# Optimization experiments

Hardware: AMD Instinct MI355X
Metric: run time of the kernel (lower is better)

The kernel has to match this reference:

```python
import jax, jax.numpy as jnp
import numpy as np

B, N, C, F = 8, 2048, 256, 128

def setup_inputs() -> dict:
    key = jax.random.key(0)
    ks = jax.random.split(key, 5)
    s = 0.02
    return {
        "x": jax.random.normal(ks[0], (B, N, C), dtype=jnp.float32),
        "Wf": jax.random.normal(ks[1], (C, F), dtype=jnp.float32) * s,
        "bf": jnp.zeros((F,), jnp.float32),
        "Wg": jax.random.normal(ks[2], (C, F), dtype=jnp.float32) * s,
        "bg": jnp.zeros((F,), jnp.float32),
        "Wh": jax.random.normal(ks[3], (C, F), dtype=jnp.float32) * s,
        "bh": jnp.zeros((F,), jnp.float32),
        "Wv": jax.random.normal(ks[4], (F, F), dtype=jnp.float32) * s,
        "bv": jnp.zeros((F,), jnp.float32),
    }

def reference(x, Wf, bf, Wg, bg, Wh, bh, Wv, bv):
    # 1x1 Conv1D == pointwise dense projection
    fx = x @ Wf + bf            # [B, N, F]
    gx = x @ Wg + bg            # [B, N, F]
    hx = x @ Wh + bh            # [B, N, F]
    # alpha = softmax(fx @ gx^T) over last axis -> [B, N, N]
    alpha = jax.nn.softmax(jnp.einsum('bnf,bmf->bnm', fx, gx), axis=-1)
    # o = hx^T @ alpha -> [B, F, N]
    o = jnp.einsum('bnf,bnm->bfm', hx, alpha)
    # faithful to original: RESHAPE (not transpose) to [B, N, F]
    o = o.reshape(B, N, F)
    return o @ Wv + bv          # [B, N, F]
```

## Files before the change

kernel.cpp:

```cpp
#include <hip/hip_runtime.h>
#include <hip/hip_bf16.h>


constexpr int Bb = 8, Nn = 2048, Cc = 256, Ff = 128;
constexpr long BNF = (long)Bb * Nn * Ff;
constexpr long BN  = (long)Bb * Nn;

typedef __bf16 bf16x8 __attribute__((ext_vector_type(8)));
typedef float  f32x4  __attribute__((ext_vector_type(4)));

__device__ inline unsigned short f2bf(float x) {
    unsigned u = __float_as_uint(x);
    unsigned r = (u + 0x7fffu + ((u >> 16) & 1u)) >> 16;
    return (unsigned short)r;
}
__device__ inline float bf2f(unsigned short h) {
    return __uint_as_float(((unsigned)h) << 16);
}


__global__ __launch_bounds__(256) void k_prepw(
    const float* __restrict__ W0, const float* __restrict__ W1,
    const float* __restrict__ W2,
    ushort* __restrict__ wth, ushort* __restrict__ wtl)
{
    __shared__ float ls[64][132];
    const float* W = (blockIdx.y == 0) ? W0 : (blockIdx.y == 1) ? W1 : W2;
    const int k0 = blockIdx.x * 64;
    const int t = threadIdx.x;
    const float4* src = (const float4*)(W + (size_t)k0 * 128);
    #pragma unroll
    for (int i = 0; i < 8; ++i) {
        int idx = t + 256 * i;
        int r = idx >> 5, c4 = idx & 31;
        *(float4*)&ls[r][c4 * 4] = src[idx];
    }
    __syncthreads();
    const int f = t >> 1, half = t & 1;
    __align__(16) ushort hb[32], lb[32];
    #pragma unroll
    for (int j = 0; j < 32; ++j) {
        float v = ls[half * 32 + j][f];
        ushort h = f2bf(v);
        hb[j] = h;
        lb[j] = f2bf(v - bf2f(h));
    }
    size_t base = ((size_t)blockIdx.y * 128 + f) * 256 + k0 + half * 32;
    #pragma unroll
    for (int j = 0; j < 4; ++j) {
        *(uint4*)&wth[base + j * 8] = *(const uint4*)&hb[j * 8];
        *(uint4*)&wtl[base + j * 8] = *(const uint4*)&lb[j * 8];
    }
}

__global__ __launch_bounds__(256) void k_prepwv(
    const float* __restrict__ Wv,
    ushort* __restrict__ wvth, ushort* __restrict__ wvtl)
{
    __shared__ float ls[64][132];
    const int k0 = blockIdx.x * 64;
    const int t = threadIdx.x;
    const float4* src = (const float4*)(Wv + (size_t)k0 * 128);
    #pragma unroll
    for (int i = 0; i < 8; ++i) {
        int idx = t + 256 * i;
        int r = idx >> 5, c4 = idx & 31;
        *(float4*)&ls[r][c4 * 4] = src[idx];
    }
    __syncthreads();
    const int f = t >> 1, half = t & 1;
    __align__(16) ushort hb[32], lb[32];
    #pragma unroll
    for (int j = 0; j < 32; ++j) {
        float v = ls[half * 32 + j][f];
        ushort h = f2bf(v);
        hb[j] = h;
        lb[j] = f2bf(v - bf2f(h));
    }
    size_t base = (size_t)f * 128 + k0 + half * 32;
    #pragma unroll
    for (int j = 0; j < 4; ++j) {
        *(uint4*)&wvth[base + j * 8] = *(const uint4*)&hb[j * 8];
        *(uint4*)&wvtl[base + j * 8] = *(const uint4*)&lb[j * 8];
    }
}

__global__ __launch_bounds__(512) void k_projm2(
    const float* __restrict__ x,
    const ushort* __restrict__ wth, const ushort* __restrict__ wtl,
    const float* __restrict__ b0, const float* __restrict__ b1,
    const float* __restrict__ b2,
    ushort* __restrict__ fxh, ushort* __restrict__ fxl,
    ushort* __restrict__ gxh, ushort* __restrict__ gxl,
    float* __restrict__ hxt)
{
    __shared__ ushort xsh[64][264], xsl[64][264];
    __shared__ float pmf[64][132];
    ushort (*pm)[136] = (ushort(*)[136])pmf;

    const int t = threadIdx.x;
    const long row0 = (long)blockIdx.x * 64;
    const int wid = t >> 6, lane = t & 63;
    const int wy = wid & 1, wx = wid >> 1;
    const int col = lane & 15, quad = lane >> 4;

    {
        #pragma unroll
        for (int i = 0; i < 8; ++i) {
            int idx = t + 512 * i;
            int r = idx >> 6, c4 = idx & 63;
            float4 v = *(const float4*)&x[(row0 + r) * 256 + c4 * 4];
            ushort4 h, l;
            h.x = f2bf(v.x); l.x = f2bf(v.x - bf2f(h.x));
            h.y = f2bf(v.y); l.y = f2bf(v.y - bf2f(h.y));
            h.z = f2bf(v.z); l.z = f2bf(v.z - bf2f(h.z));
            h.w = f2bf(v.w); l.w = f2bf(v.w - bf2f(h.w));
            *(ushort4*)&xsh[r][c4 * 4] = h;
            *(ushort4*)&xsl[r][c4 * 4] = l;
        }
    }
    __syncthreads();

    for (int y = 0; y < 3; ++y) {
        const ushort* Wh = wth + (size_t)y * 128 * 256;
        const ushort* Wl = wtl + (size_t)y * 128 * 256;
        const float* bias = (y == 0) ? b0 : (y == 1) ? b1 : b2;

        f32x4 acc[2][2];
        #pragma unroll
        for (int i = 0; i < 2; ++i)
            #pragma unroll
            for (int j = 0; j < 2; ++j) acc[i][j] = (f32x4){0.f, 0.f, 0.f, 0.f};

        #pragma unroll
        for (int kk = 0; kk < 8; ++kk) {
            const int ko = kk * 32 + quad * 8;
            bf16x8 ah[2], al[2], bh[2], bl[2];
            #pragma unroll
            for (int tn = 0; tn < 2; ++tn) {
                int r = wy * 32 + tn * 16 + col;
                ah[tn] = *(const bf16x8*)&xsh[r][ko];
                al[tn] = *(const bf16x8*)&xsl[r][ko];
            }
            #pragma unroll
            for (int tf = 0; tf < 2; ++tf) {
                int f = wx * 32 + tf * 16 + col;
                bh[tf] = *(const bf16x8*)&Wh[(size_t)f * 256 + ko];
                bl[tf] = *(const bf16x8*)&Wl[(size_t)f * 256 + ko];
            }
            #pragma unroll
            for (int tn = 0; tn < 2; ++tn)
                #pragma unroll
                for (int tf = 0; tf < 2; ++tf) {
                    acc[tn][tf] = __builtin_amdgcn_mfma_f32_16x16x32_bf16(ah[tn], bh[tf], acc[tn][tf], 0, 0, 0);
                    acc[tn][tf] = __builtin_amdgcn_mfma_f32_16x16x32_bf16(ah[tn], bl[tf], acc[tn][tf], 0, 0, 0);
                    acc[tn][tf] = __builtin_amdgcn_mfma_f32_16x16x32_bf16(al[tn], bh[tf], acc[tn][tf], 0, 0, 0);
                }
        }

        float v[2][2][4];
        #pragma unroll
        for (int tf = 0; tf < 2; ++tf) {
            float bb = bias[wx * 32 + tf * 16 + col];
            #pragma unroll
            for (int tn = 0; tn < 2; ++tn)
                #pragma unroll
                for (int r = 0; r < 4; ++r) v[tn][tf][r] = acc[tn][tf][r] + bb;
        }

        if (y == 2) {
            float* ob = hxt + (row0 >> 11) * (size_t)128 * 2048;
            int n0 = (int)(row0 & 2047);
            #pragma unroll
            for (int tn = 0; tn < 2; ++tn) {
                int n = n0 + wy * 32 + tn * 16 + quad * 4;
                #pragma unroll
                for (int tf = 0; tf < 2; ++tf) {
                    int f = wx * 32 + tf * 16 + col;
                    f32x4 vv = {v[tn][tf][0], v[tn][tf][1], v[tn][tf][2], v[tn][tf][3]};
                    *(f32x4*)&ob[(size_t)f * 2048 + n] = vv;
                }
            }
        } else {
            ushort* oh = (y == 0) ? fxh : gxh;
            ushort* ol = (y == 0) ? fxl : gxl;
            __syncthreads();
            #pragma unroll
            for (int tn = 0; tn < 2; ++tn)
                #pragma unroll
                for (int tf = 0; tf < 2; ++tf)
                    #pragma unroll
                    for (int r = 0; r < 4; ++r)
                        pm[wy * 32 + tn * 16 + quad * 4 + r][wx * 32 + tf * 16 + col] = f2bf(v[tn][tf][r]);
            __syncthreads();
            #pragma unroll
            for (int i = 0; i < 2; ++i) {
                int idx = t + 512 * i;
                int r = idx >> 4, c = idx & 15;
                *(uint4*)&oh[(row0 + r) * 128 + c * 8] = *(const uint4*)&pm[r][c * 8];
            }
            __syncthreads();
            #pragma unroll
            for (int tn = 0; tn < 2; ++tn)
                #pragma unroll
                for (int tf = 0; tf < 2; ++tf)
                    #pragma unroll
                    for (int r = 0; r < 4; ++r) {
                        float hv = bf2f(f2bf(v[tn][tf][r]));
                        pm[wy * 32 + tn * 16 + quad * 4 + r][wx * 32 + tf * 16 + col] = f2bf(v[tn][tf][r] - hv);
                    }
            __syncthreads();
            #pragma unroll
            for (int i = 0; i < 2; ++i) {
                int idx = t + 512 * i;
                int r = idx >> 4, c = idx & 15;
                *(uint4*)&ol[(row0 + r) * 128 + c * 8] = *(const uint4*)&pm[r][c * 8];
            }
            __syncthreads();
        }
    }
}

__global__ __launch_bounds__(512, 4) void k_score5(
    const ushort* __restrict__ fxh, const ushort* __restrict__ fxl,
    const ushort* __restrict__ gxh, const ushort* __restrict__ gxl,
    ushort* __restrict__ Pt, float* __restrict__ lsum2)
{
    __shared__ ushort gsh[64][136], gsl[64][136];
    __shared__ __align__(16) ushort fsbuf[2 * 64 * 136];
    __shared__ float lsum[64];
    ushort* fsh = fsbuf;
    ushort* fsl = fsbuf + 64 * 136;
    ushort* pm  = fsbuf;

    const int t = threadIdx.x;
    const int n0g = blockIdx.x * 64;
    const int ms = blockIdx.y;
    const int b = n0g >> 11;
    const int n0 = n0g & 2047;
    const int wid = t >> 6, lane = t & 63;
    const int wy = wid & 1, wx = wid >> 1;
    const int col = lane & 15, quad = lane >> 4;

    {
        const uint4* sh = (const uint4*)(fxh + (size_t)n0g * 128);
        const uint4* sl = (const uint4*)(fxl + (size_t)n0g * 128);
        #pragma unroll
        for (int i = 0; i < 2; ++i) {
            int idx = t + 512 * i;
            int r = idx >> 4, c = idx & 15;
            *(uint4*)&fsh[r * 136 + c * 8] = sh[idx];
            *(uint4*)&fsl[r * 136 + c * 8] = sl[idx];
        }
        if (t < 64) lsum[t] = 0.f;
    }
    __syncthreads();

    bf16x8 Ah[4][2], Al[4][2];
    #pragma unroll
    for (int kk = 0; kk < 4; ++kk) {
        const int ko = kk * 32 + quad * 8;
        #pragma unroll
        for (int tn = 0; tn < 2; ++tn) {
            int r = wy * 32 + tn * 16 + col;
            Ah[kk][tn] = *(const bf16x8*)&fsh[r * 136 + ko];
            Al[kk][tn] = *(const bf16x8*)&fsl[r * 136 + ko];
        }
    }

    float rs[2][4] = {};
    const ushort* gbh = gxh + (size_t)b * 2048 * 128;
    const ushort* gbl = gxl + (size_t)b * 2048 * 128;
    ushort* Pb = Pt + (size_t)b * 2048 * 2048;

    for (int mt = 0; mt < 16; ++mt) {
        const int m0 = ms * 1024 + mt * 64;
        __syncthreads();
        {
            const uint4* sh = (const uint4*)(gbh + (size_t)m0 * 128);
            const uint4* sl = (const uint4*)(gbl + (size_t)m0 * 128);
            #pragma unroll
            for (int i = 0; i < 2; ++i) {
                int idx = t + 512 * i;
                int r = idx >> 4, c = idx & 15;
                *(uint4*)&gsh[r][c * 8] = sh[idx];
                *(uint4*)&gsl[r][c * 8] = sl[idx];
            }
        }
        __syncthreads();

        f32x4 acc[2];
        acc[0] = (f32x4){0.f, 0.f, 0.f, 0.f};
        acc[1] = (f32x4){0.f, 0.f, 0.f, 0.f};

        #pragma unroll
        for (int kk = 0; kk < 4; ++kk) {
            const int ko = kk * 32 + quad * 8;
            int r = wx * 16 + col;
            bf16x8 bh = *(const bf16x8*)&gsh[r][ko];
            bf16x8 bl = *(const bf16x8*)&gsl[r][ko];
            #pragma unroll
            for (int tn = 0; tn < 2; ++tn) {
                acc[tn] = __builtin_amdgcn_mfma_f32_16x16x32_bf16(Ah[kk][tn], bh, acc[tn], 0, 0, 0);
                acc[tn] = __builtin_amdgcn_mfma_f32_16x16x32_bf16(Ah[kk][tn], bl, acc[tn], 0, 0, 0);
                acc[tn] = __builtin_amdgcn_mfma_f32_16x16x32_bf16(Al[kk][tn], bh, acc[tn], 0, 0, 0);
            }
        }

        #pragma unroll
        for (int tn = 0; tn < 2; ++tn) {
            float e0 = __expf(acc[tn][0]);
            float e1 = __expf(acc[tn][1]);
            float e2 = __expf(acc[tn][2]);
            float e3 = __expf(acc[tn][3]);
            rs[tn][0] += e0; rs[tn][1] += e1; rs[tn][2] += e2; rs[tn][3] += e3;
            ushort4 pk;
            pk.x = f2bf(e0); pk.y = f2bf(e1); pk.z = f2bf(e2); pk.w = f2bf(e3);
            int ml = wx * 16 + col;
            int nl = wy * 32 + tn * 16 + quad * 4;
            *(ushort4*)&pm[ml * 72 + nl] = pk;
        }
        __syncthreads();
        {
            int r = t >> 3, c = t & 7;
            *(uint4*)&Pb[(size_t)(m0 + r) * 2048 + n0 + c * 8] = *(const uint4*)&pm[r * 72 + c * 8];
        }
    }

    #pragma unroll
    for (int off = 1; off < 16; off <<= 1)
        #pragma unroll
        for (int tn = 0; tn < 2; ++tn)
            #pragma unroll
            for (int r = 0; r < 4; ++r) rs[tn][r] += __shfl_xor(rs[tn][r], off);
    if (col == 0) {
        #pragma unroll
        for (int tn = 0; tn < 2; ++tn)
            #pragma unroll
            for (int r = 0; r < 4; ++r)
                atomicAdd(&lsum[wy * 32 + tn * 16 + quad * 4 + r], rs[tn][r]);
    }
    __syncthreads();
    if (t < 64) lsum2[(size_t)ms * BN + n0g + t] = lsum[t];
}

__global__ __launch_bounds__(256) void k_linv(
    const float* __restrict__ lsum2, float* __restrict__ linv)
{
    const long i = (long)blockIdx.x * 256 + threadIdx.x;
    linv[i] = 1.0f / (lsum2[i] + lsum2[BN + i]);
}

__global__ __launch_bounds__(256, 2) void k_pv7b(
    const ushort* __restrict__ Pt,
    const float* __restrict__ hxt, const float* __restrict__ linv,
    float* __restrict__ op0, float* __restrict__ op1,
    float* __restrict__ op2, float* __restrict__ op3)
{
    __shared__ ushort ps[128][72];
    __shared__ ushort hsh[128][72], hsl[128][72];
    const int t = threadIdx.x;
    const int ks = blockIdx.x & 3;
    const int m0g = (blockIdx.x >> 2) * 128;
    const int b = m0g >> 11, m0 = m0g & 2047;
    const int wx = t >> 6;
    const int lane = t & 63;
    const int col = lane & 15, quad = lane >> 4;
    const int nbase = ks * 512;

    const ushort* Pb = Pt + ((size_t)b * 2048 + m0) * 2048 + nbase;
    const float* Hx = hxt + (size_t)b * 128 * 2048 + nbase;
    const float* Lv = linv + (size_t)b * 2048 + nbase;

    f32x4 acc[8][2];
    #pragma unroll
    for (int i = 0; i < 8; ++i)
        #pragma unroll
        for (int j = 0; j < 2; ++j) acc[i][j] = (f32x4){0.f, 0.f, 0.f, 0.f};

    for (int nt = 0; nt < 8; ++nt) {
        __syncthreads();
        {
            #pragma unroll
            for (int i = 0; i < 4; ++i) {
                int idx = t + 256 * i;
                int r = idx >> 3, c = idx & 7;
                size_t g = (size_t)r * 2048 + nt * 64 + c * 8;
                *(uint4*)&ps[r][c * 8] = *(const uint4*)&Pb[g];
                float4 h0 = *(const float4*)&Hx[g];
                float4 h1 = *(const float4*)&Hx[g + 4];
                float4 l0 = *(const float4*)&Lv[nt * 64 + c * 8];
                float4 l1 = *(const float4*)&Lv[nt * 64 + c * 8 + 4];
                float w[8] = {h0.x * l0.x, h0.y * l0.y, h0.z * l0.z, h0.w * l0.w,
                              h1.x * l1.x, h1.y * l1.y, h1.z * l1.z, h1.w * l1.w};
                __align__(16) ushort hb[8], lb[8];
                #pragma unroll
                for (int j = 0; j < 8; ++j) {
                    ushort h = f2bf(w[j]);
                    hb[j] = h;
                    lb[j] = f2bf(w[j] - bf2f(h));
                }
                *(uint4*)&hsh[r][c * 8] = *(const uint4*)&hb[0];
                *(uint4*)&hsl[r][c * 8] = *(const uint4*)&lb[0];
            }
        }
        __syncthreads();

        #pragma unroll
        for (int kk = 0; kk < 2; ++kk) {
            const int ko = kk * 32 + quad * 8;
            bf16x8 a[8], bh[2], bl[2];
            #pragma unroll
            for (int tm = 0; tm < 8; ++tm)
                a[tm] = *(const bf16x8*)&ps[tm * 16 + col][ko];
            #pragma unroll
            for (int tf = 0; tf < 2; ++tf) {
                int r = wx * 32 + tf * 16 + col;
                bh[tf] = *(const bf16x8*)&hsh[r][ko];
                bl[tf] = *(const bf16x8*)&hsl[r][ko];
            }
            #pragma unroll
            for (int tm = 0; tm < 8; ++tm)
                #pragma unroll
                for (int tf = 0; tf < 2; ++tf) {
                    acc[tm][tf] = __builtin_amdgcn_mfma_f32_16x16x32_bf16(a[tm], bh[tf], acc[tm][tf], 0, 0, 0);
                    acc[tm][tf] = __builtin_amdgcn_mfma_f32_16x16x32_bf16(a[tm], bl[tf], acc[tm][tf], 0, 0, 0);
                }
        }
    }

    float* op = (ks == 0) ? op0 : (ks == 1) ? op1 : (ks == 2) ? op2 : op3;
    float* ob = op + (size_t)b * 128 * 2048;
    #pragma unroll
    for (int tm = 0; tm < 8; ++tm) {
        int m = m0 + tm * 16 + quad * 4;
        #pragma unroll
        for (int tf = 0; tf < 2; ++tf) {
            int f = wx * 32 + tf * 16 + col;
            *(f32x4*)&ob[(size_t)f * 2048 + m] = acc[tm][tf];
        }
    }
}

__global__ __launch_bounds__(512) void k_final_m3(
    const float* __restrict__ op0, const float* __restrict__ op1,
    const float* __restrict__ op2, const float* __restrict__ op3,
    const ushort* __restrict__ wvth, const ushort* __restrict__ wvtl,
    const float* __restrict__ bv, float* __restrict__ out)
{
    __shared__ ushort ash[64][136], asl[64][136];
    __shared__ float pmf[64][132];
    const int t = threadIdx.x;
    const long row0 = (long)blockIdx.x * 64;
    const int wid = t >> 6, lane = t & 63;
    const int wy = wid & 1, wx = wid >> 1;
    const int col = lane & 15, quad = lane >> 4;

    {
        const float4* s0 = (const float4*)(op0 + row0 * 128);
        const float4* s1 = (const float4*)(op1 + row0 * 128);
        const float4* s2 = (const float4*)(op2 + row0 * 128);
        const float4* s3 = (const float4*)(op3 + row0 * 128);
        #pragma unroll
        for (int i = 0; i < 4; ++i) {
            int idx = t + 512 * i;
            float4 a = s0[idx], bq = s1[idx], cq = s2[idx], dq = s3[idx];
            float v0 = ((a.x + bq.x) + cq.x) + dq.x;
            float v1 = ((a.y + bq.y) + cq.y) + dq.y;
            float v2 = ((a.z + bq.z) + cq.z) + dq.z;
            float v3 = ((a.w + bq.w) + cq.w) + dq.w;
            ushort4 h, l;
            h.x = f2bf(v0); l.x = f2bf(v0 - bf2f(h.x));
            h.y = f2bf(v1); l.y = f2bf(v1 - bf2f(h.y));
            h.z = f2bf(v2); l.z = f2bf(v2 - bf2f(h.z));
            h.w = f2bf(v3); l.w = f2bf(v3 - bf2f(h.w));
            int r = idx >> 5, c4 = idx & 31;
            *(ushort4*)&ash[r][c4 * 4] = h;
            *(ushort4*)&asl[r][c4 * 4] = l;
        }
    }
    __syncthreads();

    f32x4 acc[2][2];
    #pragma unroll
    for (int i = 0; i < 2; ++i)
        #pragma unroll
        for (int j = 0; j < 2; ++j) acc[i][j] = (f32x4){0.f, 0.f, 0.f, 0.f};

    #pragma unroll
    for (int kk = 0; kk < 4; ++kk) {
        const int ko = kk * 32 + quad * 8;
        bf16x8 ah[2], al[2], bh[2], bl[2];
        #pragma unroll
        for (int tn = 0; tn < 2; ++tn) {
            int r = wy * 32 + tn * 16 + col;
            ah[tn] = *(const bf16x8*)&ash[r][ko];
            al[tn] = *(const bf16x8*)&asl[r][ko];
        }
        #pragma unroll
        for (int tf = 0; tf < 2; ++tf) {
            int f = wx * 32 + tf * 16 + col;
            bh[tf] = *(const bf16x8*)&wvth[(size_t)f * 128 + ko];
            bl[tf] = *(const bf16x8*)&wvtl[(size_t)f * 128 + ko];
        }
        #pragma unroll
        for (int tn = 0; tn < 2; ++tn)
            #pragma unroll
            for (int tf = 0; tf < 2; ++tf) {
                acc[tn][tf] = __builtin_amdgcn_mfma_f32_16x16x32_bf16(ah[tn], bh[tf], acc[tn][tf], 0, 0, 0);
                acc[tn][tf] = __builtin_amdgcn_mfma_f32_16x16x32_bf16(ah[tn], bl[tf], acc[tn][tf], 0, 0, 0);
                acc[tn][tf] = __builtin_amdgcn_mfma_f32_16x16x32_bf16(al[tn], bh[tf], acc[tn][tf], 0, 0, 0);
            }
    }

    #pragma unroll
    for (int tf = 0; tf < 2; ++tf) {
        int f = wx * 32 + tf * 16 + col;
        float bb = bv[f];
        #pragma unroll
        for (int tn = 0; tn < 2; ++tn)
            #pragma unroll
            for (int r = 0; r < 4; ++r)
                pmf[wy * 32 + tn * 16 + quad * 4 + r][f] = acc[tn][tf][r] + bb;
    }
    __syncthreads();
    #pragma unroll
    for (int i = 0; i < 4; ++i) {
        int idx = t + 512 * i;
        int r = idx >> 5, c4 = idx & 31;
        *(float4*)&out[(row0 + r) * 128 + c4 * 4] = *(const float4*)&pmf[r][c4 * 4];
    }
}


__global__ __launch_bounds__(256) void k_proj(
    const float* __restrict__ x,
    const float* __restrict__ W0, const float* __restrict__ b0,
    const float* __restrict__ W1, const float* __restrict__ b1,
    const float* __restrict__ W2, const float* __restrict__ b2,
    float* __restrict__ o0, float* __restrict__ o1, float* __restrict__ o2)
{
    const float* W; const float* bias; float* out;
    if (blockIdx.y == 0)      { W = W0; bias = b0; out = o0; }
    else if (blockIdx.y == 1) { W = W1; bias = b1; out = o1; }
    else                      { W = W2; bias = b2; out = o2; }

    __shared__ float xs[32][Cc];
    const int t = threadIdx.x;
    const long row0 = (long)blockIdx.x * 32;
    const float4* xg = (const float4*)(x + row0 * Cc);
    float4* xs4 = (float4*)xs;
    #pragma unroll
    for (int i = 0; i < 8; ++i) xs4[t + 256 * i] = xg[t + 256 * i];
    __syncthreads();

    const int cg = t & 31;
    const int rq = t >> 5;
    float acc[4][4] = {};
    const float4* W4 = (const float4*)W;
    for (int k4 = 0; k4 < Cc / 4; ++k4) {
        float4 av[4];
        #pragma unroll
        for (int i = 0; i < 4; ++i) av[i] = *(const float4*)&xs[4 * rq + i][k4 * 4];
        float4 wv4[4];
        #pragma unroll
        for (int kk = 0; kk < 4; ++kk) wv4[kk] = W4[(size_t)(4 * k4 + kk) * (Ff / 4) + cg];
        #pragma unroll
        for (int kk = 0; kk < 4; ++kk) {
            float4 w = wv4[kk];
            #pragma unroll
            for (int i = 0; i < 4; ++i) {
                float a = (kk == 0) ? av[i].x : (kk == 1) ? av[i].y : (kk == 2) ? av[i].z : av[i].w;
                acc[i][0] += a * w.x; acc[i][1] += a * w.y;
                acc[i][2] += a * w.z; acc[i][3] += a * w.w;
            }
        }
    }
    float4 bb = ((const float4*)bias)[cg];
    #pragma unroll
    for (int i = 0; i < 4; ++i) {
        float4 r;
        r.x = acc[i][0] + bb.x; r.y = acc[i][1] + bb.y;
        r.z = acc[i][2] + bb.z; r.w = acc[i][3] + bb.w;
        ((float4*)(out + (row0 + 4 * rq + i) * Ff))[cg] = r;
    }
}

__global__ __launch_bounds__(256) void k_stats(
    const float* __restrict__ fx, const float* __restrict__ gx,
    float* __restrict__ linv)
{
    __shared__ float fs[64][132];
    __shared__ float gs[128][132];
    const int t = threadIdx.x;
    const int n0 = blockIdx.x * 64;
    const int b = n0 / Nn;
    const float* gxb = gx + (long)b * Nn * Ff;
    {
        const float4* src = (const float4*)(fx + (long)n0 * Ff);
        #pragma unroll
        for (int i = 0; i < 8; ++i) {
            int idx = t + 256 * i;
            int r = idx >> 5, c4 = idx & 31;
            *(float4*)&fs[r][c4 * 4] = src[idx];
        }
    }
    const int ty = t >> 4;
    const int tx = t & 15;
    float lsum[4] = {0.f, 0.f, 0.f, 0.f};
    for (int mt = 0; mt < Nn / 128; ++mt) {
        __syncthreads();
        {
            const float4* src = (const float4*)(gxb + (long)mt * 128 * Ff);
            #pragma unroll
            for (int i = 0; i < 16; ++i) {
                int idx = t + 256 * i;
                int r = idx >> 5, c4 = idx & 31;
                *(float4*)&gs[r][c4 * 4] = src[idx];
            }
        }
        __syncthreads();
        float s[4][8] = {};
        for (int k4 = 0; k4 < 32; ++k4) {
            float4 a[4], g4[8];
            #pragma unroll
            for (int i = 0; i < 4; ++i) a[i] = *(const float4*)&fs[ty + 16 * i][k4 * 4];
            #pragma unroll
            for (int j = 0; j < 8; ++j) g4[j] = *(const float4*)&gs[tx + 16 * j][k4 * 4];
            #pragma unroll
            for (int i = 0; i < 4; ++i)
                #pragma unroll
                for (int j = 0; j < 8; ++j)
                    s[i][j] += a[i].x * g4[j].x + a[i].y * g4[j].y
                             + a[i].z * g4[j].z + a[i].w * g4[j].w;
        }
        #pragma unroll
        for (int i = 0; i < 4; ++i) {
            float e = 0.f;
            #pragma unroll
            for (int j = 0; j < 8; ++j) e += __expf(s[i][j]);
            lsum[i] += e;
        }
    }
    #pragma unroll
    for (int off = 1; off < 16; off <<= 1)
        #pragma unroll
        for (int i = 0; i < 4; ++i) lsum[i] += __shfl_xor(lsum[i], off);
    if (tx == 0)
        #pragma unroll
        for (int i = 0; i < 4; ++i) linv[n0 + ty + 16 * i] = 1.0f / lsum[i];
}

__global__ __launch_bounds__(256) void k_attnpv(
    const float* __restrict__ fx, const float* __restrict__ gx,
    const float* __restrict__ hx, const float* __restrict__ linv,
    float* __restrict__ o)
{
    __shared__ float gs[64][132];
    __shared__ float fs[64][132];
    __shared__ float hs[64][132];
    __shared__ float ps[64][68];
    __shared__ float li[64];
    const int t = threadIdx.x;
    const int m0g = blockIdx.x * 64;
    const int b = m0g / Nn;
    const int m0 = m0g - b * Nn;
    const float* fxb = fx + (long)b * Nn * Ff;
    const float* hxb = hx + (long)b * Nn * Ff;
    {
        const float4* src = (const float4*)(gx + (long)m0g * Ff);
        #pragma unroll
        for (int i = 0; i < 8; ++i) {
            int idx = t + 256 * i;
            int r = idx >> 5, c4 = idx & 31;
            *(float4*)&gs[r][c4 * 4] = src[idx];
        }
    }
    const int ty = t >> 4;
    const int tx = t & 15;
    float acc[4][8] = {};
    for (int nt = 0; nt < Nn / 64; ++nt) {
        __syncthreads();
        {
            const float4* srcf = (const float4*)(fxb + (long)nt * 64 * Ff);
            const float4* srch = (const float4*)(hxb + (long)nt * 64 * Ff);
            #pragma unroll
            for (int i = 0; i < 8; ++i) {
                int idx = t + 256 * i;
                int r = idx >> 5, c4 = idx & 31;
                *(float4*)&fs[r][c4 * 4] = srcf[idx];
                *(float4*)&hs[r][c4 * 4] = srch[idx];
            }
            if (t < 64) li[t] = linv[(long)b * Nn + nt * 64 + t];
        }
        __syncthreads();
        float s[4][4] = {};
        for (int k4 = 0; k4 < 32; ++k4) {
            float4 a[4], g4[4];
            #pragma unroll
            for (int i = 0; i < 4; ++i) a[i] = *(const float4*)&fs[ty + 16 * i][k4 * 4];
            #pragma unroll
            for (int j = 0; j < 4; ++j) g4[j] = *(const float4*)&gs[tx + 16 * j][k4 * 4];
            #pragma unroll
            for (int i = 0; i < 4; ++i)
                #pragma unroll
                for (int j = 0; j < 4; ++j)
                    s[i][j] += a[i].x * g4[j].x + a[i].y * g4[j].y
                             + a[i].z * g4[j].z + a[i].w * g4[j].w;
        }
        #pragma unroll
        for (int i = 0; i < 4; ++i) {
            float lv = li[ty + 16 * i];
            #pragma unroll
            for (int j = 0; j < 4; ++j)
                ps[ty + 16 * i][tx + 16 * j] = __expf(s[i][j]) * lv;
        }
        __syncthreads();
        #pragma unroll 4
        for (int n = 0; n < 64; ++n) {
            float4 h0 = *(const float4*)&hs[n][tx * 8];
            float4 h1 = *(const float4*)&hs[n][tx * 8 + 4];
            float pv[4];
            #pragma unroll
            for (int im = 0; im < 4; ++im) pv[im] = ps[n][ty + 16 * im];
            #pragma unroll
            for (int im = 0; im < 4; ++im) {
                acc[im][0] += pv[im] * h0.x; acc[im][1] += pv[im] * h0.y;
                acc[im][2] += pv[im] * h0.z; acc[im][3] += pv[im] * h0.w;
                acc[im][4] += pv[im] * h1.x; acc[im][5] += pv[im] * h1.y;
                acc[im][6] += pv[im] * h1.z; acc[im][7] += pv[im] * h1.w;
            }
        }
    }
    float* ob = o + (size_t)b * Ff * Nn;
    #pragma unroll
    for (int im = 0; im < 4; ++im) {
        int m = m0 + ty + 16 * im;
        #pragma unroll
        for (int jf = 0; jf < 8; ++jf)
            ob[(size_t)(tx * 8 + jf) * Nn + m] = acc[im][jf];
    }
}

__global__ __launch_bounds__(256) void k_final(
    const float* __restrict__ in2, const float* __restrict__ Wv,
    const float* __restrict__ bv, float* __restrict__ out)
{
    __shared__ float xs[32][132];
    const int t = threadIdx.x;
    const long row0 = (long)blockIdx.x * 32;
    {
        const float4* src = (const float4*)(in2 + row0 * Ff);
        #pragma unroll
        for (int i = 0; i < 4; ++i) {
            int idx = t + 256 * i;
            int r = idx >> 5, c4 = idx & 31;
            *(float4*)&xs[r][c4 * 4] = src[idx];
        }
    }
    __syncthreads();

    const int cg = t & 31;
    const int rq = t >> 5;
    float acc[4][4] = {};
    const float4* W4 = (const float4*)Wv;
    for (int k4 = 0; k4 < 32; ++k4) {
        float4 av[4];
        #pragma unroll
        for (int i = 0; i < 4; ++i) av[i] = *(const float4*)&xs[4 * rq + i][k4 * 4];
        float4 wv4[4];
        #pragma unroll
        for (int kk = 0; kk < 4; ++kk) wv4[kk] = W4[(size_t)(4 * k4 + kk) * 32 + cg];
        #pragma unroll
        for (int kk = 0; kk < 4; ++kk) {
            float4 w = wv4[kk];
            #pragma unroll
            for (int i = 0; i < 4; ++i) {
                float a = (kk == 0) ? av[i].x : (kk == 1) ? av[i].y : (kk == 2) ? av[i].z : av[i].w;
                acc[i][0] += a * w.x; acc[i][1] += a * w.y;
                acc[i][2] += a * w.z; acc[i][3] += a * w.w;
            }
        }
    }
    float4 bb = ((const float4*)bv)[cg];
    #pragma unroll
    for (int i = 0; i < 4; ++i) {
        float4 r;
        r.x = acc[i][0] + bb.x; r.y = acc[i][1] + bb.y;
        r.z = acc[i][2] + bb.z; r.w = acc[i][3] + bb.w;
        ((float4*)(out + (row0 + 4 * rq + i) * Ff))[cg] = r;
    }
}


extern "C" void kernel_launch(void* const* d_in, const int* in_sizes, int n_in,
                              void* d_out, int out_size, void* d_ws, size_t ws_size,
                              hipStream_t stream) {
    const float* x  = (const float*)d_in[0];
    const float* Wf = (const float*)d_in[1];
    const float* bf = (const float*)d_in[2];
    const float* Wg = (const float*)d_in[3];
    const float* bg = (const float*)d_in[4];
    const float* Wh = (const float*)d_in[5];
    const float* bh = (const float*)d_in[6];
    const float* Wv = (const float*)d_in[7];
    const float* bv = (const float*)d_in[8];
    float* out = (float*)d_out;

    const size_t sz_hxt  = (size_t)BNF * 4;
    const size_t sz_linv = (size_t)BN * 4;
    const size_t sz_bf   = (size_t)BNF * 2;
    const size_t sz_Pt   = (size_t)Bb * Nn * Nn * 2;
    const size_t sz_wt   = (size_t)3 * 128 * 256 * 2;
    const size_t sz_wv   = (size_t)128 * 128 * 2;
    const size_t need = sz_hxt + sz_linv + 8 * sz_bf + sz_Pt + 2 * sz_wt + 2 * sz_wv;

    if (ws_size >= need) {
        char* p = (char*)d_ws;
        float* hxt   = (float*)p;            p += sz_hxt;
        float* linv  = (float*)p;            p += sz_linv;
        ushort* fxh  = (ushort*)p;           p += sz_bf;
        ushort* fxl  = (ushort*)p;           p += sz_bf;
        ushort* gxh  = (ushort*)p;           p += sz_bf;
        ushort* gxl  = (ushort*)p;           p += sz_bf;
        float* op0   = (float*)p;            p += 2 * sz_bf;
        float* lsum2 = (float*)p;
        float* op3   = (float*)p;
        float* op1   = (float*)fxh;
        float* op2   = (float*)gxh;
        p += 2 * sz_bf;
        ushort* wth  = (ushort*)p;           p += sz_wt;
        ushort* wtl  = (ushort*)p;           p += sz_wt;
        ushort* wvth = (ushort*)p;           p += sz_wv;
        ushort* wvtl = (ushort*)p;           p += sz_wv;
        ushort* Pt   = (ushort*)p;

        k_prepw   <<<dim3(4, 3), 256, 0, stream>>>(Wf, Wg, Wh, wth, wtl);
        k_prepwv  <<<2, 256, 0, stream>>>(Wv, wvth, wvtl);
        k_projm2  <<<BN / 64, 512, 0, stream>>>(x, wth, wtl, bf, bg, bh,
                                                fxh, fxl, gxh, gxl, hxt);
        k_score5  <<<dim3(BN / 64, 2), 512, 0, stream>>>(fxh, fxl, gxh, gxl, Pt, lsum2);
        k_linv    <<<BN / 256, 256, 0, stream>>>(lsum2, linv);
        k_pv7b    <<<(BN / 128) * 4, 256, 0, stream>>>(Pt, hxt, linv, op0, op1, op2, op3);
        k_final_m3<<<BN / 64, 512, 0, stream>>>(op0, op1, op2, op3, wvth, wvtl, bv, out);
    } else {
        float* ws   = (float*)d_ws;
        float* fx   = ws;
        float* gx   = fx + BNF;
        float* hx   = gx + BNF;
        float* linv = hx + BNF;
        float* o    = linv + BN;
        k_proj  <<<dim3(BN / 32, 3), 256, 0, stream>>>(x, Wf, bf, Wg, bg, Wh, bh, fx, gx, hx);
        k_stats <<<BN / 64, 256, 0, stream>>>(fx, gx, linv);
        k_attnpv<<<BN / 64, 256, 0, stream>>>(fx, gx, hx, linv, o);
        k_final <<<BN / 32, 256, 0, stream>>>(o, Wv, bv, out);
    }
}
```

Baseline: 188.9 us.

## Pack weights in MFMA fragment order and split projection K into two LDS chunks

Weight prep kernels now write the bf16 hi/lo split weights in a per-lane MFMA fragment layout, so each lane loads one contiguous 16-byte chunk per tile. The projection kernel stages x in two 128-wide K chunks, which halves its LDS footprint, and keeps all three projection accumulators live so x is converted only once per chunk. It also adds an occupancy hint and drops one barrier. The aim is coalesced weight loads and higher occupancy, at the cost of more accumulator registers and an extra sync between chunks.

Result: faster. 177.6 us (median of 2 runs) (-6.0%).

```diff
diff --git a/kernel.cpp b/kernel.cpp
--- a/kernel.cpp
+++ b/kernel.cpp
@@ -19,10 +19,10 @@
 }
 
 
-__global__ __launch_bounds__(256) void k_prepw(
+__global__ __launch_bounds__(256) void k_prepw2(
     const float* __restrict__ W0, const float* __restrict__ W1,
     const float* __restrict__ W2,
-    ushort* __restrict__ wth, ushort* __restrict__ wtl)
+    ushort* __restrict__ wpkh, ushort* __restrict__ wpkl)
 {
     __shared__ float ls[64][132];
     const float* W = (blockIdx.y == 0) ? W0 : (blockIdx.y == 1) ? W1 : W2;
@@ -36,26 +36,32 @@
         *(float4*)&ls[r][c4 * 4] = src[idx];
     }
     __syncthreads();
-    const int f = t >> 1, half = t & 1;
-    __align__(16) ushort hb[32], lb[32];
-    #pragma unroll
-    for (int j = 0; j < 32; ++j) {
-        float v = ls[half * 32 + j][f];
-        ushort h = f2bf(v);
-        hb[j] = h;
-        lb[j] = f2bf(v - bf2f(h));
-    }
-    size_t base = ((size_t)blockIdx.y * 128 + f) * 256 + k0 + half * 32;
-    #pragma unroll
-    for (int j = 0; j < 4; ++j) {
-        *(uint4*)&wth[base + j * 8] = *(const uint4*)&hb[j * 8];
-        *(uint4*)&wtl[base + j * 8] = *(const uint4*)&lb[j * 8];
-    }
-}
-
-__global__ __launch_bounds__(256) void k_prepwv(
+    const int lane = t & 63, grp = t >> 6;
+    const int col = lane & 15, quad = lane >> 4;
+    const int kc = blockIdx.x >> 1;
+    const int kkb = (blockIdx.x & 1) * 2;
+    #pragma unroll
+    for (int g = grp; g < 16; g += 4) {
+        int kk_sub = g >> 3;
+        int ft = g & 7;
+        int f = ft * 16 + col;
+        __align__(16) ushort hb[8], lb[8];
+        #pragma unroll
+        for (int j = 0; j < 8; ++j) {
+            float v = ls[kk_sub * 32 + quad * 8 + j][f];
+            ushort h = f2bf(v);
+            hb[j] = h;
+            lb[j] = f2bf(v - bf2f(h));
+        }
+        size_t base = ((((size_t)blockIdx.y * 2 + kc) * 4 + (kkb + kk_sub)) * 8 + ft) * 512 + (size_t)lane * 8;
+        *(uint4*)&wpkh[base] = *(const uint4*)&hb[0];
+        *(uint4*)&wpkl[base] = *(const uint4*)&lb[0];
+    }
+}
+
+__global__ __launch_bounds__(256) void k_prepwv2(
     const float* __restrict__ Wv,
-    ushort* __restrict__ wvth, ushort* __restrict__ wvtl)
+    ushort* __restrict__ wvpkh, ushort* __restrict__ wvpkl)
 {
     __shared__ float ls[64][132];
     const int k0 = blockIdx.x * 64;
@@ -68,35 +74,38 @@
         *(float4*)&ls[r][c4 * 4] = src[idx];
     }
     __syncthreads();
-    const int f = t >> 1, half = t & 1;
-    __align__(16) ushort hb[32], lb[32];
-    #pragma unroll
-    for (int j = 0; j < 32; ++j) {
-        float v = ls[half * 32 + j][f];
-        ushort h = f2bf(v);
-        hb[j] = h;
-        lb[j] = f2bf(v - bf2f(h));
-    }
-    size_t base = (size_t)f * 128 + k0 + half * 32;
-    #pragma unroll
-    for (int j = 0; j < 4; ++j) {
-        *(uint4*)&wvth[base + j * 8] = *(const uint4*)&hb[j * 8];
-        *(uint4*)&wvtl[base + j * 8] = *(const uint4*)&lb[j * 8];
-    }
-}
-
-__global__ __launch_bounds__(512) void k_projm2(
+    const int lane = t & 63, grp = t >> 6;
+    const int col = lane & 15, quad = lane >> 4;
+    #pragma unroll
+    for (int g = grp; g < 16; g += 4) {
+        int kk_sub = g >> 3;
+        int ft = g & 7;
+        int f = ft * 16 + col;
+        __align__(16) ushort hb[8], lb[8];
+        #pragma unroll
+        for (int j = 0; j < 8; ++j) {
+            float v = ls[kk_sub * 32 + quad * 8 + j][f];
+            ushort h = f2bf(v);
+            hb[j] = h;
+            lb[j] = f2bf(v - bf2f(h));
+        }
+        size_t base = (((size_t)(blockIdx.x * 2 + kk_sub)) * 8 + ft) * 512 + (size_t)lane * 8;
+        *(uint4*)&wvpkh[base] = *(const uint4*)&hb[0];
+        *(uint4*)&wvpkl[base] = *(const uint4*)&lb[0];
+    }
+}
+
+__global__ __launch_bounds__(512, 4) void k_projm2b(
     const float* __restrict__ x,
-    const ushort* __restrict__ wth, const ushort* __restrict__ wtl,
+    const ushort* __restrict__ wpkh, const ushort* __restrict__ wpkl,
     const float* __restrict__ b0, const float* __restrict__ b1,
     const float* __restrict__ b2,
     ushort* __restrict__ fxh, ushort* __restrict__ fxl,
     ushort* __restrict__ gxh, ushort* __restrict__ gxl,
     float* __restrict__ hxt)
 {
-    __shared__ ushort xsh[64][264], xsl[64][264];
-    __shared__ float pmf[64][132];
-    ushort (*pm)[136] = (ushort(*)[136])pmf;
+    __shared__ ushort xsh[64][136], xsl[64][136];
+    __shared__ ushort pm[64][136];
 
     const int t = threadIdx.x;
     const long row0 = (long)blockIdx.x * 64;
@@ -104,60 +113,66 @@
     const int wy = wid & 1, wx = wid >> 1;
     const int col = lane & 15, quad = lane >> 4;
 
-    {
-        #pragma unroll
-        for (int i = 0; i < 8; ++i) {
-            int idx = t + 512 * i;
-            int r = idx >> 6, c4 = idx & 63;
-            float4 v = *(const float4*)&x[(row0 + r) * 256 + c4 * 4];
-            ushort4 h, l;
-            h.x = f2bf(v.x); l.x = f2bf(v.x - bf2f(h.x));
-            h.y = f2bf(v.y); l.y = f2bf(v.y - bf2f(h.y));
-            h.z = f2bf(v.z); l.z = f2bf(v.z - bf2f(h.z));
-            h.w = f2bf(v.w); l.w = f2bf(v.w - bf2f(h.w));
-            *(ushort4*)&xsh[r][c4 * 4] = h;
-            *(ushort4*)&xsl[r][c4 * 4] = l;
-        }
-    }
-    __syncthreads();
-
+    f32x4 acc[3][2][2];
+    #pragma unroll
+    for (int y = 0; y < 3; ++y)
+        #pragma unroll
+        for (int i = 0; i < 2; ++i)
+            #pragma unroll
+            for (int j = 0; j < 2; ++j) acc[y][i][j] = (f32x4){0.f, 0.f, 0.f, 0.f};
+
+    for (int kc = 0; kc < 2; ++kc) {
+        if (kc) __syncthreads();
+        {
+            #pragma unroll
+            for (int i = 0; i < 4; ++i) {
+                int idx = t + 512 * i;
+                int r = idx >> 5, c4 = idx & 31;
+                float4 v = *(const float4*)&x[(row0 + r) * 256 + kc * 128 + c4 * 4];
+                ushort4 h, l;
+                h.x = f2bf(v.x); l.x = f2bf(v.x - bf2f(h.x));
+                h.y = f2bf(v.y); l.y = f2bf(v.y - bf2f(h.y));
+                h.z = f2bf(v.z); l.z = f2bf(v.z - bf2f(h.z));
+                h.w = f2bf(v.w); l.w = f2bf(v.w - bf2f(h.w));
+                *(ushort4*)&xsh[r][c4 * 4] = h;
+                *(ushort4*)&xsl[r][c4 * 4] = l;
+            }
+        }
+        __syncthreads();
+
+        #pragma unroll
+        for (int y = 0; y < 3; ++y) {
+            #pragma unroll
+            for (int kk = 0; kk < 4; ++kk) {
+                const int ko = kk * 32 + quad * 8;
+                bf16x8 ah[2], al[2], bh[2], bl[2];
+                #pragma unroll
+                for (int tn = 0; tn < 2; ++tn) {
+                    int r = wy * 32 + tn * 16 + col;
+                    ah[tn] = *(const bf16x8*)&xsh[r][ko];
+                    al[tn] = *(const bf16x8*)&xsl[r][ko];
+                }
+                #pragma unroll
+                for (int tf = 0; tf < 2; ++tf) {
+                    size_t base = ((((size_t)y * 2 + kc) * 4 + kk) * 8 + (wx * 2 + tf)) * 512 + (size_t)lane * 8;
+                    bh[tf] = *(const bf16x8*)&wpkh[base];
+                    bl[tf] = *(const bf16x8*)&wpkl[base];
+                }
+                #pragma unroll
+                for (int tn = 0; tn < 2; ++tn)
+                    #pragma unroll
+                    for (int tf = 0; tf < 2; ++tf) {
+                        acc[y][tn][tf] = __builtin_amdgcn_mfma_f32_16x16x32_bf16(ah[tn], bh[tf], acc[y][tn][tf], 0, 0, 0);
+                        acc[y][tn][tf] = __builtin_amdgcn_mfma_f32_16x16x32_bf16(ah[tn], bl[tf], acc[y][tn][tf], 0, 0, 0);
+                        acc[y][tn][tf] = __builtin_amdgcn_mfma_f32_16x16x32_bf16(al[tn], bh[tf], acc[y][tn][tf], 0, 0, 0);
+                    }
+            }
+        }
+    }
+
+    #pragma unroll
     for (int y = 0; y < 3; ++y) {
-        const ushort* Wh = wth + (size_t)y * 128 * 256;
-        const ushort* Wl = wtl + (size_t)y * 128 * 256;
         const float* bias = (y == 0) ? b0 : (y == 1) ? b1 : b2;
-
-        f32x4 acc[2][2];
-        #pragma unroll
-        for (int i = 0; i < 2; ++i)
-            #pragma unroll
-            for (int j = 0; j < 2; ++j) acc[i][j] = (f32x4){0.f, 0.f, 0.f, 0.f};
-
-        #pragma unroll
-        for (int kk = 0; kk < 8; ++kk) {
-            const int ko = kk * 32 + quad * 8;
-            bf16x8 ah[2], al[2], bh[2], bl[2];
-            #pragma unroll
-            for (int tn = 0; tn < 2; ++tn) {
-                int r = wy * 32 + tn * 16 + col;
-                ah[tn] = *(const bf16x8*)&xsh[r][ko];
-                al[tn] = *(const bf16x8*)&xsl[r][ko];
-            }
-            #pragma unroll
-            for (int tf = 0; tf < 2; ++tf) {
-                int f = wx * 32 + tf * 16 + col;
-                bh[tf] = *(const bf16x8*)&Wh[(size_t)f * 256 + ko];
-                bl[tf] = *(const bf16x8*)&Wl[(size_t)f * 256 + ko];
-            }
-            #pragma unroll
-            for (int tn = 0; tn < 2; ++tn)
-                #pragma unroll
-                for (int tf = 0; tf < 2; ++tf) {
-                    acc[tn][tf] = __builtin_amdgcn_mfma_f32_16x16x32_bf16(ah[tn], bh[tf], acc[tn][tf], 0, 0, 0);
-                    acc[tn][tf] = __builtin_amdgcn_mfma_f32_16x16x32_bf16(ah[tn], bl[tf], acc[tn][tf], 0, 0, 0);
-                    acc[tn][tf] = __builtin_amdgcn_mfma_f32_16x16x32_bf16(al[tn], bh[tf], acc[tn][tf], 0, 0, 0);
-                }
-        }
-
         float v[2][2][4];
         #pragma unroll
         for (int tf = 0; tf < 2; ++tf) {
@@ -165,7 +180,7 @@
             #pragma unroll
             for (int tn = 0; tn < 2; ++tn)
                 #pragma unroll
-                for (int r = 0; r < 4; ++r) v[tn][tf][r] = acc[tn][tf][r] + bb;
+                for (int r = 0; r < 4; ++r) v[tn][tf][r] = acc[y][tn][tf][r] + bb;
         }
 
         if (y == 2) {
@@ -184,7 +199,7 @@
         } else {
             ushort* oh = (y == 0) ? fxh : gxh;
             ushort* ol = (y == 0) ? fxl : gxl;
-            __syncthreads();
+            if (y == 0) __syncthreads();
             #pragma unroll
             for (int tn = 0; tn < 2; ++tn)
                 #pragma unroll
@@ -442,10 +457,10 @@
     }
 }
 
-__global__ __launch_bounds__(512) void k_final_m3(
+__global__ __launch_bounds__(512) void k_final_m3b(
     const float* __restrict__ op0, const float* __restrict__ op1,
     const float* __restrict__ op2, const float* __restrict__ op3,
-    const ushort* __restrict__ wvth, const ushort* __restrict__ wvtl,
+    const ushort* __restrict__ wvpkh, const ushort* __restrict__ wvpkl,
     const float* __restrict__ bv, float* __restrict__ out)
 {
     __shared__ ushort ash[64][136], asl[64][136];
@@ -499,9 +514,9 @@
         }
         #pragma unroll
         for (int tf = 0; tf < 2; ++tf) {
-            int f = wx * 32 + tf * 16 + col;
-            bh[tf] = *(const bf16x8*)&wvth[(size_t)f * 128 + ko];
-            bl[tf] = *(const bf16x8*)&wvtl[(size_t)f * 128 + ko];
+            size_t base = (((size_t)kk) * 8 + (wx * 2 + tf)) * 512 + (size_t)lane * 8;
+            bh[tf] = *(const bf16x8*)&wvpkh[base];
+            bl[tf] = *(const bf16x8*)&wvpkl[base];
         }
         #pragma unroll
         for (int tn = 0; tn < 2; ++tn)
@@ -829,20 +844,20 @@
         float* op1   = (float*)fxh;
         float* op2   = (float*)gxh;
         p += 2 * sz_bf;
-        ushort* wth  = (ushort*)p;           p += sz_wt;
-        ushort* wtl  = (ushort*)p;           p += sz_wt;
-        ushort* wvth = (ushort*)p;           p += sz_wv;
-        ushort* wvtl = (ushort*)p;           p += sz_wv;
-        ushort* Pt   = (ushort*)p;
-
-        k_prepw   <<<dim3(4, 3), 256, 0, stream>>>(Wf, Wg, Wh, wth, wtl);
-        k_prepwv  <<<2, 256, 0, stream>>>(Wv, wvth, wvtl);
-        k_projm2  <<<BN / 64, 512, 0, stream>>>(x, wth, wtl, bf, bg, bh,
+        ushort* wpkh  = (ushort*)p;          p += sz_wt;
+        ushort* wpkl  = (ushort*)p;          p += sz_wt;
+        ushort* wvpkh = (ushort*)p;          p += sz_wv;
+        ushort* wvpkl = (ushort*)p;          p += sz_wv;
+        ushort* Pt    = (ushort*)p;
+
+        k_prepw2  <<<dim3(4, 3), 256, 0, stream>>>(Wf, Wg, Wh, wpkh, wpkl);
+        k_prepwv2 <<<2, 256, 0, stream>>>(Wv, wvpkh, wvpkl);
+        k_projm2b <<<BN / 64, 512, 0, stream>>>(x, wpkh, wpkl, bf, bg, bh,
                                                 fxh, fxl, gxh, gxl, hxt);
         k_score5  <<<dim3(BN / 64, 2), 512, 0, stream>>>(fxh, fxl, gxh, gxl, Pt, lsum2);
         k_linv    <<<BN / 256, 256, 0, stream>>>(lsum2, linv);
         k_pv7b    <<<(BN / 128) * 4, 256, 0, stream>>>(Pt, hxt, linv, op0, op1, op2, op3);
-        k_final_m3<<<BN / 64, 512, 0, stream>>>(op0, op1, op2, op3, wvth, wvtl, bv, out);
+        k_final_m3b<<<BN / 64, 512, 0, stream>>>(op0, op1, op2, op3, wvpkh, wvpkl, bv, out);
     } else {
         float* ws   = (float*)d_ws;
         float* fx   = ws;
```
